# Kernel optimization log

Hardware: AMD Instinct MI355X
Metric: run time of the kernel (lower is better)

The kernel has to match this reference:

```python
import jax, jax.numpy as jnp
import numpy as np

L, N, E, H, R = 2048, 4, 768, 12, 16
ALPHA = 16.0
LORA_SCALE = ALPHA / R
HEAD_DIM = E // H


def setup_inputs() -> dict:
    rng = jax.random.key(0)
    ks = jax.random.split(rng, 15)
    g = lambda i, shape, s=1.0: jax.random.normal(ks[i], shape, jnp.float32) * s
    return {
        "query": g(0, (L, N, E)),
        "key": g(1, (L, N, E)),
        "value": g(2, (L, N, E)),
        "in_proj_weight": g(3, (3 * E, E), 0.02),
        "in_proj_bias": g(4, (3 * E,), 0.02),
        "q_down": g(5, (R, E), 0.02),
        "q_up": g(6, (E, R), 0.02),
        "k_down": g(7, (R, E), 0.02),
        "k_up": g(8, (E, R), 0.02),
        "v_down": g(9, (R, E), 0.02),
        "v_up": g(10, (E, R), 0.02),
        "out_proj_weight": g(11, (E, E), 0.02),
        "out_proj_bias": g(12, (E,), 0.02),
        "out_down": g(13, (R, E), 0.02),
        "out_up": g(14, (E, R), 0.02),
    }


def _lora_linear(x, W, b, down, up):
    # y = x W^T + b + scale * (x down^T) up^T   (LoRA-adapted nn.Linear)
    return x @ W.T + b + LORA_SCALE * ((x @ down.T) @ up.T)


def reference(query, key, value, in_proj_weight, in_proj_bias,
              q_down, q_up, k_down, k_up, v_down, v_up,
              out_proj_weight, out_proj_bias, out_down, out_up):
    Wq, Wk, Wv = jnp.split(in_proj_weight, 3, axis=0)
    bq, bk, bv = jnp.split(in_proj_bias, 3)
    q = _lora_linear(query, Wq, bq, q_down, q_up)   # (L,N,E)
    k = _lora_linear(key, Wk, bk, k_down, k_up)     # (S,N,E)
    v = _lora_linear(value, Wv, bv, v_down, v_up)

    def to_heads(t):  # (T,N,E) -> (N,H,T,hd)
        return t.reshape(t.shape[0], N, H, HEAD_DIM).transpose(1, 2, 0, 3)

    qh, kh, vh = to_heads(q), to_heads(k), to_heads(v)
    scale = 1.0 / jnp.sqrt(jnp.float32(HEAD_DIM))
    scores = jnp.einsum('nhld,nhsd->nhls', qh * scale, kh)  # (N,H,L,S)
    attn = jax.nn.softmax(scores, axis=-1)
    o = jnp.einsum('nhls,nhsd->nhld', attn, vh)             # (N,H,L,hd)
    o = o.transpose(2, 0, 1, 3).reshape(L, N, E)            # (L,N,E)
    return _lora_linear(o, out_proj_weight, out_proj_bias, out_down, out_up)
```

## Files before the change

kernel.cpp:

```cpp
#include <hip/hip_runtime.h>

#define LL 2048
#define NN 4
#define EE 768
#define HH 12
#define RR 16
#define HD 64
#define TT (LL*NN)
#define F3 (3*EE)
#define KA 832

typedef __bf16 bf16;
typedef bf16 bf16x4 __attribute__((ext_vector_type(4)));
typedef bf16 bf16x8 __attribute__((ext_vector_type(8)));
typedef float floatx4 __attribute__((ext_vector_type(4)));

__global__ __launch_bounds__(256) void cast_x(
    const float* __restrict__ q, const float* __restrict__ k,
    const float* __restrict__ v, bf16* __restrict__ Xa)
{
    const int bid = blockIdx.x;
    const int third = bid / (TT/8);
    const int r0 = (bid % (TT/8)) * 8;
    const float* x = (third == 0) ? q : (third == 1) ? k : v;
    const int tid = threadIdx.x;
    #pragma unroll
    for (int i = 0; i < 6; ++i) {
        const int e4 = i*256 + tid;
        const int row = e4 / 192;
        const int col = (e4 % 192) * 4;
        const float4 f = *(const float4*)(x + (size_t)(r0+row)*EE + col);
        bf16x4 h = { (bf16)f.x, (bf16)f.y, (bf16)f.z, (bf16)f.w };
        *(bf16x4*)(Xa + ((size_t)third*TT + r0 + row)*KA + col) = h;
    }
}

__global__ __launch_bounds__(256) void prep_w(
    const float* __restrict__ W,  const float* __restrict__ qu,
    const float* __restrict__ ku, const float* __restrict__ vu,
    const float* __restrict__ Wo, const float* __restrict__ ou,
    const float* __restrict__ qd, const float* __restrict__ kd,
    const float* __restrict__ vd, const float* __restrict__ odw,
    bf16* __restrict__ Wa, bf16* __restrict__ Dm)
{
    const int f = blockIdx.x;
    const int tid = threadIdx.x;
    if (f < 3072) {
        const float* src;
        const float* up;
        if (f < F3) {
            const int third = f / EE, fe = f % EE;
            src = W + (size_t)f*EE;
            up  = ((third == 0) ? qu : (third == 1) ? ku : vu) + fe*RR;
        } else {
            const int fe = f - F3;
            src = Wo + (size_t)fe*EE;
            up  = ou + fe*RR;
        }
        bf16* row = Wa + (size_t)f*KA;
        #pragma unroll
        for (int i = 0; i < 3; ++i)
            row[i*256 + tid] = (bf16)src[i*256 + tid];
        if (tid < 64)
            row[EE + tid] = (tid < RR) ? (bf16)up[tid] : (bf16)0.f;
    } else {
        const int f2 = f - 3072;
        const int which = f2 >> 4, r = f2 & 15;
        const float* dsrc = (which == 0) ? qd : (which == 1) ? kd
                          : (which == 2) ? vd : odw;
        bf16* drow = Dm + (size_t)f2*EE;
        #pragma unroll
        for (int i = 0; i < 3; ++i)
            drow[i*256 + tid] = (bf16)dsrc[(size_t)r*EE + i*256 + tid];
    }
}

template<int XA>
__global__ __launch_bounds__(256) void lora_rank16(
    bf16* __restrict__ A, const bf16* __restrict__ Dm)
{
    __shared__ float red[4][64][16];
    const int row0 = blockIdx.x * 64;
    const int dn = XA ? (row0 >> 13) : 3;
    const bf16* D = Dm + (size_t)dn*16*EE;
    const int tid = threadIdx.x;
    const int wave = tid >> 6, lane = tid & 63;
    const int quad = lane >> 4, l16 = lane & 15;

    floatx4 acc[4];
    #pragma unroll
    for (int rt = 0; rt < 4; ++rt) acc[rt] = (floatx4){0.f,0.f,0.f,0.f};

    #pragma unroll
    for (int ks = 0; ks < 6; ++ks) {
        const int k0 = wave*192 + ks*32;
        const bf16x8 b = *(const bf16x8*)(D + (size_t)l16*EE + k0 + quad*8);
        #pragma unroll
        for (int rt = 0; rt < 4; ++rt) {
            const bf16x8 a = *(const bf16x8*)(
                A + (size_t)(row0 + rt*16 + l16)*KA + k0 + quad*8);
            acc[rt] = __builtin_amdgcn_mfma_f32_16x16x32_bf16(a, b, acc[rt], 0, 0, 0);
        }
    }

    #pragma unroll
    for (int rt = 0; rt < 4; ++rt)
        #pragma unroll
        for (int rr = 0; rr < 4; ++rr)
            red[wave][rt*16 + quad*4 + rr][l16] = acc[rt][rr];
    __syncthreads();

    {
        const int row = tid >> 2, cq = (tid & 3) * 4;
        bf16x4 o;
        #pragma unroll
        for (int j = 0; j < 4; ++j) {
            const float s = red[0][row][cq+j] + red[1][row][cq+j]
                          + red[2][row][cq+j] + red[3][row][cq+j];
            o[j] = (bf16)s;
        }
        *(bf16x4*)(A + (size_t)(row0+row)*KA + EE + cq) = o;
    }
    #pragma unroll
    for (int p = 0; p < 3; ++p) {
        const int id = p*256 + tid;
        const int row = id / 12, c = id % 12;
        *(bf16x4*)(A + (size_t)(row0+row)*KA + 784 + c*4) = (bf16x4){};
    }
}

template<int MODE>
__global__ __launch_bounds__(256) void gemm_aug(
    const bf16* __restrict__ A,
    const bf16* __restrict__ B,
    const float* __restrict__ bias,
    bf16* __restrict__ qo, bf16* __restrict__ ko, bf16* __restrict__ vo,
    float* __restrict__ fo)
{
    __shared__ bf16 As[128][72];
    __shared__ bf16 Bs[128][72];
    const int t0 = blockIdx.x * 128;
    const int f0 = blockIdx.y * 128;
    const int tid = threadIdx.x;
    const int wave = tid >> 6, lane = tid & 63;
    const int quad = lane >> 4, l16 = lane & 15;
    const int m0 = (wave & 1) * 64;
    const int n0 = (wave >> 1) * 64;

    const int third = (MODE == 0) ? (f0 / EE) : 0;
    const bf16* Aeff = (MODE == 0) ? (A + (size_t)third*TT*KA) : A;

    floatx4 acc[4][4];
    #pragma unroll
    for (int rt = 0; rt < 4; ++rt)
        #pragma unroll
        for (int ct = 0; ct < 4; ++ct) acc[rt][ct] = (floatx4){0.f,0.f,0.f,0.f};

    for (int kb = 0; kb < KA/64; ++kb) {
        __syncthreads();
        #pragma unroll
        for (int c = 0; c < 4; ++c) {
            int id = c*256 + tid;
            int row = id >> 3, cg = id & 7;
            *(bf16x8*)(&As[row][cg*8]) =
                *(const bf16x8*)(Aeff + (size_t)(t0+row)*KA + kb*64 + cg*8);
            *(bf16x8*)(&Bs[row][cg*8]) =
                *(const bf16x8*)(B + (size_t)(f0+row)*KA + kb*64 + cg*8);
        }
        __syncthreads();
        #pragma unroll
        for (int kc = 0; kc < 2; ++kc) {
            bf16x8 a[4], bfr[4];
            #pragma unroll
            for (int rt = 0; rt < 4; ++rt)
                a[rt] = *(const bf16x8*)(&As[m0 + rt*16 + l16][kc*32 + quad*8]);
            #pragma unroll
            for (int ct = 0; ct < 4; ++ct)
                bfr[ct] = *(const bf16x8*)(&Bs[n0 + ct*16 + l16][kc*32 + quad*8]);
            #pragma unroll
            for (int rt = 0; rt < 4; ++rt)
                #pragma unroll
                for (int ct = 0; ct < 4; ++ct)
                    acc[rt][ct] = __builtin_amdgcn_mfma_f32_16x16x32_bf16(
                        a[rt], bfr[ct], acc[rt][ct], 0, 0, 0);
        }
    }

    #pragma unroll
    for (int rt = 0; rt < 4; ++rt) {
        #pragma unroll
        for (int r = 0; r < 4; ++r) {
            const int t = t0 + m0 + rt*16 + quad*4 + r;
            #pragma unroll
            for (int ct = 0; ct < 4; ++ct) {
                const int fl = n0 + ct*16 + l16;
                float c = acc[rt][ct][r] + bias[f0 + fl];
                if (MODE == 0) {
                    const int fe = (f0 % EE) + fl;
                    const int h = fe >> 6, d = fe & 63;
                    const int l = t >> 2, n = t & 3;
                    const size_t idx = (((size_t)(n*HH + h)*LL) + l)*HD + d;
                    if (third == 0)      qo[idx] = (bf16)(c * 0.180336877f);
                    else if (third == 1) ko[idx] = (bf16)c;
                    else                 vo[idx] = (bf16)c;
                } else {
                    fo[(size_t)t*EE + f0 + fl] = c;
                }
            }
        }
    }
}

__global__ __launch_bounds__(256) void vtrans(
    const bf16* __restrict__ vin, bf16* __restrict__ vout)
{
    __shared__ bf16 T[64][64];
    const int nh = blockIdx.x >> 5;
    const int l0 = (blockIdx.x & 31) * 64;
    const int tid = threadIdx.x;
    const bf16* src = vin + ((size_t)nh*LL + l0)*HD;
    #pragma unroll
    for (int c = 0; c < 2; ++c) {
        int id = c*256 + tid;
        int row = id >> 3, dg = id & 7;
        int pg = dg ^ (row & 7);
        *(bf16x8*)(&T[row][pg*8]) = *(const bf16x8*)(src + row*HD + dg*8);
    }
    __syncthreads();
    bf16* dst = vout + (size_t)nh*HD*LL;
    const int wave = tid >> 6, lane = tid & 63;
    #pragma unroll
    for (int it = 0; it < 2; ++it) {
        const int d  = it*32 + wave*8 + (lane >> 3);
        const int cg = lane & 7;
        bf16x8 vv;
        #pragma unroll
        for (int j = 0; j < 8; ++j) {
            const int lrow = cg*8 + j;
            const int pg = (d >> 3) ^ (lrow & 7);
            vv[j] = T[lrow][pg*8 + (d & 7)];
        }
        *(bf16x8*)(dst + (size_t)d*LL + l0 + cg*8) = vv;
    }
}

__global__ __launch_bounds__(256) void attn_mfma(
    const bf16* __restrict__ qf, const bf16* __restrict__ kf,
    const bf16* __restrict__ vf, bf16* __restrict__ Oa)
{
    __shared__ bf16 Ks[64][72];
    __shared__ bf16 Vt[64][72];
    __shared__ bf16 Ps[128][72];

    const int bid = blockIdx.x;
    const int nh = bid % 48;
    const int l0 = (bid / 48) * 128;
    const int tid  = threadIdx.x;
    const int wave = tid >> 6;
    const int lane = tid & 63;
    const int quad = lane >> 4;
    const int l16  = lane & 15;
    const int m0   = wave * 32;

    const bf16* qb = qf + (size_t)nh * LL * HD;
    const bf16* kb = kf + (size_t)nh * LL * HD;
    const bf16* vb = vf + (size_t)nh * HD * LL;

    bf16x8 aq[2][2];
    #pragma unroll
    for (int kc = 0; kc < 2; ++kc)
        #pragma unroll
        for (int rt = 0; rt < 2; ++rt)
            aq[kc][rt] = *(const bf16x8*)(
                qb + (size_t)(l0 + m0 + rt*16 + l16)*HD + kc*32 + quad*8);

    floatx4 oacc[2][4];
    float lrow[2][4];
    #pragma unroll
    for (int rt = 0; rt < 2; ++rt)
        #pragma unroll
        for (int ct = 0; ct < 4; ++ct) oacc[rt][ct] = (floatx4){0.f,0.f,0.f,0.f};
    #pragma unroll
    for (int rt = 0; rt < 2; ++rt)
        #pragma unroll
        for (int r = 0; r < 4; ++r) lrow[rt][r] = 0.f;

    for (int s0 = 0; s0 < LL; s0 += 64) {
        __syncthreads();
        #pragma unroll
        for (int it = 0; it < 2; ++it) {
            int lin  = it*256 + tid;
            int row  = lin >> 3;
            int colg = (lin & 7) * 8;
            *(bf16x8*)(&Ks[row][colg]) =
                *(const bf16x8*)(kb + (size_t)(s0+row)*HD + colg);
            *(bf16x8*)(&Vt[row][colg]) =
                *(const bf16x8*)(vb + (size_t)row*LL + s0 + colg);
        }
        __syncthreads();

        floatx4 sf[2][4];
        #pragma unroll
        for (int rt = 0; rt < 2; ++rt)
            #pragma unroll
            for (int ct = 0; ct < 4; ++ct) sf[rt][ct] = (floatx4){0.f,0.f,0.f,0.f};
        #pragma unroll
        for (int kc = 0; kc < 2; ++kc) {
            bf16x8 bk[4];
            #pragma unroll
            for (int ct = 0; ct < 4; ++ct)
                bk[ct] = *(const bf16x8*)(&Ks[ct*16 + l16][kc*32 + quad*8]);
            #pragma unroll
            for (int rt = 0; rt < 2; ++rt)
                #pragma unroll
                for (int ct = 0; ct < 4; ++ct)
                    sf[rt][ct] = __builtin_amdgcn_mfma_f32_16x16x32_bf16(
                        aq[kc][rt], bk[ct], sf[rt][ct], 0, 0, 0);
        }

        #pragma unroll
        for (int rt = 0; rt < 2; ++rt) {
            #pragma unroll
            for (int r = 0; r < 4; ++r) {
                const int prow = m0 + rt*16 + quad*4 + r;
                float ps = 0.f;
                #pragma unroll
                for (int ct = 0; ct < 4; ++ct) {
                    const float p = __builtin_exp2f(sf[rt][ct][r]);
                    Ps[prow][ct*16 + l16] = (bf16)p;
                    ps += p;
                }
                lrow[rt][r] += ps;
            }
        }

        #pragma unroll
        for (int kc = 0; kc < 2; ++kc) {
            bf16x8 ap[2], bv[4];
            ap[0] = *(const bf16x8*)(&Ps[m0      + l16][kc*32 + quad*8]);
            ap[1] = *(const bf16x8*)(&Ps[m0 + 16 + l16][kc*32 + quad*8]);
            #pragma unroll
            for (int ct = 0; ct < 4; ++ct)
                bv[ct] = *(const bf16x8*)(&Vt[ct*16 + l16][kc*32 + quad*8]);
            #pragma unroll
            for (int rt = 0; rt < 2; ++rt)
                #pragma unroll
                for (int ct = 0; ct < 4; ++ct)
                    oacc[rt][ct] = __builtin_amdgcn_mfma_f32_16x16x32_bf16(
                        ap[rt], bv[ct], oacc[rt][ct], 0, 0, 0);
        }
    }

    #pragma unroll
    for (int rt = 0; rt < 2; ++rt)
        #pragma unroll
        for (int r = 0; r < 4; ++r) {
            float s = lrow[rt][r];
            #pragma unroll
            for (int off = 1; off < 16; off <<= 1)
                s += __shfl_xor(s, off, 64);
            lrow[rt][r] = s;
        }

    const int n = nh / HH, h = nh % HH;
    #pragma unroll
    for (int rt = 0; rt < 2; ++rt) {
        #pragma unroll
        for (int r = 0; r < 4; ++r) {
            const float inv = 1.f / lrow[rt][r];
            const int lq = l0 + m0 + rt*16 + quad*4 + r;
            const size_t t = (size_t)lq*NN + n;
            #pragma unroll
            for (int ct = 0; ct < 4; ++ct)
                Oa[t*KA + h*64 + ct*16 + l16] = (bf16)(oacc[rt][ct][r] * inv);
        }
    }
}

extern "C" void kernel_launch(void* const* d_in, const int* in_sizes, int n_in,
                              void* d_out, int out_size, void* d_ws, size_t ws_size,
                              hipStream_t stream) {
    const float* q   = (const float*)d_in[0];
    const float* k   = (const float*)d_in[1];
    const float* v   = (const float*)d_in[2];
    const float* W   = (const float*)d_in[3];
    const float* b   = (const float*)d_in[4];
    const float* qd  = (const float*)d_in[5];
    const float* qu  = (const float*)d_in[6];
    const float* kd  = (const float*)d_in[7];
    const float* ku  = (const float*)d_in[8];
    const float* vd  = (const float*)d_in[9];
    const float* vu  = (const float*)d_in[10];
    const float* Wo  = (const float*)d_in[11];
    const float* bo  = (const float*)d_in[12];
    const float* odw = (const float*)d_in[13];
    const float* ou  = (const float*)d_in[14];
    float* out = (float*)d_out;

    char* wsb = (char*)d_ws;
    bf16* Xa  = (bf16*)wsb;
    bf16* vfb = (bf16*)wsb;
    bf16* Oa  = (bf16*)(wsb + (size_t)TT*EE*2);
    bf16* Wa  = (bf16*)(wsb + (size_t)3*TT*KA*2);
    bf16* qfb = (bf16*)((char*)Wa + (size_t)3072*KA*2);
    bf16* kfb = qfb + (size_t)TT*EE;
    bf16* vld = kfb + (size_t)TT*EE;
    bf16* Dm  = vld + (size_t)TT*EE;

    cast_x<<<3072, 256, 0, stream>>>(q, k, v, Xa);
    prep_w<<<3136, 256, 0, stream>>>(W, qu, ku, vu, Wo, ou, qd, kd, vd, odw, Wa, Dm);
    lora_rank16<1><<<3*TT/64, 256, 0, stream>>>(Xa, Dm);
    gemm_aug<0><<<dim3(TT/128, F3/128), 256, 0, stream>>>(
        Xa, Wa, b, qfb, kfb, vld, nullptr);
    vtrans<<<48*32, 256, 0, stream>>>(vld, vfb);
    attn_mfma<<<48*16, 256, 0, stream>>>(qfb, kfb, vfb, Oa);
    lora_rank16<0><<<TT/64, 256, 0, stream>>>(Oa, Dm);
    gemm_aug<1><<<dim3(TT/128, EE/128), 256, 0, stream>>>(
        Oa, Wa + (size_t)F3*KA, bo, nullptr, nullptr, nullptr, out);
}
```

Before: 324.0 us.

## Keep softmax probabilities in registers using transposed 32x32 MFMA attention

```diff
diff --git a/kernel.cpp b/kernel.cpp
--- a/kernel.cpp
+++ b/kernel.cpp
@@ -14,6 +14,8 @@
 typedef bf16 bf16x4 __attribute__((ext_vector_type(4)));
 typedef bf16 bf16x8 __attribute__((ext_vector_type(8)));
 typedef float floatx4 __attribute__((ext_vector_type(4)));
+typedef float floatx16 __attribute__((ext_vector_type(16)));
+typedef unsigned uintx4 __attribute__((ext_vector_type(4)));
 
 __global__ __launch_bounds__(256) void cast_x(
     const float* __restrict__ q, const float* __restrict__ k,
@@ -244,13 +246,17 @@
     }
 }
 
+__device__ __forceinline__ unsigned pk_bf16(float a, float b) {
+    unsigned r;
+    asm("v_cvt_pk_bf16_f32 %0, %1, %2" : "=v"(r) : "v"(a), "v"(b));
+    return r;
+}
+
 __global__ __launch_bounds__(256) void attn_mfma(
     const bf16* __restrict__ qf, const bf16* __restrict__ kf,
     const bf16* __restrict__ vf, bf16* __restrict__ Oa)
 {
-    __shared__ bf16 Ks[64][72];
-    __shared__ bf16 Vt[64][72];
-    __shared__ bf16 Ps[128][72];
+    __shared__ float linv[4][32];
 
     const int bid = blockIdx.x;
     const int nh = bid % 48;
@@ -258,122 +264,96 @@
     const int tid  = threadIdx.x;
     const int wave = tid >> 6;
     const int lane = tid & 63;
-    const int quad = lane >> 4;
-    const int l16  = lane & 15;
-    const int m0   = wave * 32;
+    const int l32  = lane & 31;
+    const int hi   = lane >> 5;
 
     const bf16* qb = qf + (size_t)nh * LL * HD;
     const bf16* kb = kf + (size_t)nh * LL * HD;
     const bf16* vb = vf + (size_t)nh * HD * LL;
 
-    bf16x8 aq[2][2];
-    #pragma unroll
-    for (int kc = 0; kc < 2; ++kc)
-        #pragma unroll
-        for (int rt = 0; rt < 2; ++rt)
-            aq[kc][rt] = *(const bf16x8*)(
-                qb + (size_t)(l0 + m0 + rt*16 + l16)*HD + kc*32 + quad*8);
-
-    floatx4 oacc[2][4];
-    float lrow[2][4];
-    #pragma unroll
-    for (int rt = 0; rt < 2; ++rt)
-        #pragma unroll
-        for (int ct = 0; ct < 4; ++ct) oacc[rt][ct] = (floatx4){0.f,0.f,0.f,0.f};
-    #pragma unroll
-    for (int rt = 0; rt < 2; ++rt)
-        #pragma unroll
-        for (int r = 0; r < 4; ++r) lrow[rt][r] = 0.f;
-
-    for (int s0 = 0; s0 < LL; s0 += 64) {
-        __syncthreads();
-        #pragma unroll
-        for (int it = 0; it < 2; ++it) {
-            int lin  = it*256 + tid;
-            int row  = lin >> 3;
-            int colg = (lin & 7) * 8;
-            *(bf16x8*)(&Ks[row][colg]) =
-                *(const bf16x8*)(kb + (size_t)(s0+row)*HD + colg);
-            *(bf16x8*)(&Vt[row][colg]) =
-                *(const bf16x8*)(vb + (size_t)row*LL + s0 + colg);
-        }
-        __syncthreads();
-
-        floatx4 sf[2][4];
-        #pragma unroll
-        for (int rt = 0; rt < 2; ++rt)
+    const int q0 = l0 + wave * 32;
+
+    bf16x8 bq[4];
+    #pragma unroll
+    for (int t = 0; t < 4; ++t)
+        bq[t] = *(const bf16x8*)(qb + (size_t)(q0 + l32)*HD + t*16 + hi*8);
+
+    floatx16 oacc0 = {0,0,0,0, 0,0,0,0, 0,0,0,0, 0,0,0,0};
+    floatx16 oacc1 = {0,0,0,0, 0,0,0,0, 0,0,0,0, 0,0,0,0};
+    float lsum = 0.f;
+
+    const bf16* kp  = kb + (size_t)l32*HD + hi*8;
+    const bf16* vp0 = vb + (size_t)l32*LL + hi*8;
+    const bf16* vp1 = vb + (size_t)(32 + l32)*LL + hi*8;
+
+    bf16x8 ak[4];
+    #pragma unroll
+    for (int t = 0; t < 4; ++t)
+        ak[t] = *(const bf16x8*)(kp + t*16);
+
+    for (int s = 0; s < LL; s += 32) {
+        floatx16 sacc = {0,0,0,0, 0,0,0,0, 0,0,0,0, 0,0,0,0};
+        #pragma unroll
+        for (int t = 0; t < 4; ++t)
+            sacc = __builtin_amdgcn_mfma_f32_32x32x16_bf16(ak[t], bq[t], sacc, 0, 0, 0);
+
+        bf16x8 bv[4];
+        #pragma unroll
+        for (int tl = 0; tl < 2; ++tl) {
+            bv[tl*2+0] = *(const bf16x8*)(vp0 + s + tl*16);
+            bv[tl*2+1] = *(const bf16x8*)(vp1 + s + tl*16);
+        }
+        {
+            const int sn = (s + 32) & (LL - 1);
             #pragma unroll
-            for (int ct = 0; ct < 4; ++ct) sf[rt][ct] = (floatx4){0.f,0.f,0.f,0.f};
-        #pragma unroll
-        for (int kc = 0; kc < 2; ++kc) {
-            bf16x8 bk[4];
-            #pragma unroll
-            for (int ct = 0; ct < 4; ++ct)
-                bk[ct] = *(const bf16x8*)(&Ks[ct*16 + l16][kc*32 + quad*8]);
-            #pragma unroll
-            for (int rt = 0; rt < 2; ++rt)
-                #pragma unroll
-                for (int ct = 0; ct < 4; ++ct)
-                    sf[rt][ct] = __builtin_amdgcn_mfma_f32_16x16x32_bf16(
-                        aq[kc][rt], bk[ct], sf[rt][ct], 0, 0, 0);
-        }
-
-        #pragma unroll
-        for (int rt = 0; rt < 2; ++rt) {
-            #pragma unroll
-            for (int r = 0; r < 4; ++r) {
-                const int prow = m0 + rt*16 + quad*4 + r;
-                float ps = 0.f;
-                #pragma unroll
-                for (int ct = 0; ct < 4; ++ct) {
-                    const float p = __builtin_exp2f(sf[rt][ct][r]);
-                    Ps[prow][ct*16 + l16] = (bf16)p;
-                    ps += p;
-                }
-                lrow[rt][r] += ps;
-            }
-        }
-
-        #pragma unroll
-        for (int kc = 0; kc < 2; ++kc) {
-            bf16x8 ap[2], bv[4];
-            ap[0] = *(const bf16x8*)(&Ps[m0      + l16][kc*32 + quad*8]);
-            ap[1] = *(const bf16x8*)(&Ps[m0 + 16 + l16][kc*32 + quad*8]);
-            #pragma unroll
-            for (int ct = 0; ct < 4; ++ct)
-                bv[ct] = *(const bf16x8*)(&Vt[ct*16 + l16][kc*32 + quad*8]);
-            #pragma unroll
-            for (int rt = 0; rt < 2; ++rt)
-                #pragma unroll
-                for (int ct = 0; ct < 4; ++ct)
-                    oacc[rt][ct] = __builtin_amdgcn_mfma_f32_16x16x32_bf16(
-                        ap[rt], bv[ct], oacc[rt][ct], 0, 0, 0);
-        }
-    }
-
-    #pragma unroll
-    for (int rt = 0; rt < 2; ++rt)
-        #pragma unroll
-        for (int r = 0; r < 4; ++r) {
-            float s = lrow[rt][r];
-            #pragma unroll
-            for (int off = 1; off < 16; off <<= 1)
-                s += __shfl_xor(s, off, 64);
-            lrow[rt][r] = s;
-        }
+            for (int t = 0; t < 4; ++t)
+                ak[t] = *(const bf16x8*)(kp + (size_t)sn*HD + t*16);
+        }
+
+        float p[16];
+        #pragma unroll
+        for (int r = 0; r < 16; ++r) {
+            p[r] = __builtin_exp2f(sacc[r]);
+            lsum += p[r];
+        }
+
+        union { uintx4 u; bf16x8 h; } fr0, fr1;
+        {
+            unsigned c0 = pk_bf16(p[0], p[1]);
+            unsigned c1 = pk_bf16(p[2], p[3]);
+            unsigned c2 = pk_bf16(p[4], p[5]);
+            unsigned c3 = pk_bf16(p[6], p[7]);
+            asm("v_permlane32_swap_b32 %0, %1" : "+v"(c0), "+v"(c2));
+            asm("v_permlane32_swap_b32 %0, %1" : "+v"(c1), "+v"(c3));
+            fr0.u = (uintx4){c0, c1, c2, c3};
+        }
+        {
+            unsigned c0 = pk_bf16(p[8],  p[9]);
+            unsigned c1 = pk_bf16(p[10], p[11]);
+            unsigned c2 = pk_bf16(p[12], p[13]);
+            unsigned c3 = pk_bf16(p[14], p[15]);
+            asm("v_permlane32_swap_b32 %0, %1" : "+v"(c0), "+v"(c2));
+            asm("v_permlane32_swap_b32 %0, %1" : "+v"(c1), "+v"(c3));
+            fr1.u = (uintx4){c0, c1, c2, c3};
+        }
+
+        oacc0 = __builtin_amdgcn_mfma_f32_32x32x16_bf16(fr0.h, bv[0], oacc0, 0, 0, 0);
+        oacc1 = __builtin_amdgcn_mfma_f32_32x32x16_bf16(fr0.h, bv[1], oacc1, 0, 0, 0);
+        oacc0 = __builtin_amdgcn_mfma_f32_32x32x16_bf16(fr1.h, bv[2], oacc0, 0, 0, 0);
+        oacc1 = __builtin_amdgcn_mfma_f32_32x32x16_bf16(fr1.h, bv[3], oacc1, 0, 0, 0);
+    }
+
+    lsum += __shfl_xor(lsum, 32, 64);
+    if (lane < 32) linv[wave][l32] = 1.f / lsum;
 
     const int n = nh / HH, h = nh % HH;
     #pragma unroll
-    for (int rt = 0; rt < 2; ++rt) {
-        #pragma unroll
-        for (int r = 0; r < 4; ++r) {
-            const float inv = 1.f / lrow[rt][r];
-            const int lq = l0 + m0 + rt*16 + quad*4 + r;
-            const size_t t = (size_t)lq*NN + n;
-            #pragma unroll
-            for (int ct = 0; ct < 4; ++ct)
-                Oa[t*KA + h*64 + ct*16 + l16] = (bf16)(oacc[rt][ct][r] * inv);
-        }
+    for (int r = 0; r < 16; ++r) {
+        const int qloc = (r & 3) + 8*(r >> 2) + 4*hi;
+        const float iv = linv[wave][qloc];
+        const size_t t = (size_t)(q0 + qloc)*NN + n;
+        Oa[t*KA + h*64 + l32]      = (bf16)(oacc0[r] * iv);
+        Oa[t*KA + h*64 + 32 + l32] = (bf16)(oacc1[r] * iv);
     }
 }
 
```

Result: slower. 412.8 us (+27.4%).
